# Optimization experiments

Hardware: AMD Instinct MI355X
Metric: run time of the kernel (lower is better)

The kernel has to match this reference:

```python
import jax, jax.numpy as jnp
import numpy as np

GAMMA = 2.0  # init arg gamma
EPS = 1e-8   # torch F.cosine_similarity eps


def setup_inputs() -> dict:
    key = jax.random.key(0)
    k1, k2, k3 = jax.random.split(key, 3)
    B, C, H, W_ = 4, 256, 64, 64
    x = jax.random.normal(k1, (B, C, H, W_), dtype=jnp.float32)
    # 1x1 conv weight [out_c, in_c] and bias
    W = jax.random.normal(k2, (C, C), dtype=jnp.float32) * (1.0 / np.sqrt(C))
    b = jax.random.normal(k3, (C,), dtype=jnp.float32) * 0.01
    return {"x": x, "W": W, "b": b}


def reference(x, W, b):
    B, C, H, W_ = x.shape
    N = H * W_
    xf = x.reshape(B, C, N)                                    # [B,C,N]
    # cosine similarity across channel dim, with torch-style eps clamp
    norm = jnp.maximum(jnp.sqrt(jnp.sum(xf * xf, axis=1)), EPS)  # [B,N]
    xn = xf / norm[:, None, :]                                  # [B,C,N]
    sim = jnp.einsum('bcn,bcm->bnm', xn, xn)                    # [B,N,N]
    sim = jax.nn.relu(sim) ** GAMMA
    # 1x1 conv = per-pixel channel mixing
    t = jnp.einsum('oc,bchw->bohw', W, x) + b[None, :, None, None]
    tf = t.reshape(B, C, N)                                     # [B,C,N]
    # einsum 'b x y h w, b c h w -> b c x y'
    out = jnp.einsum('bnm,bcm->bcn', sim, tf)
    return out.reshape(B, C, H, W_)
```

## Files before the change

kernel.cpp:

```cpp
#include <hip/hip_runtime.h>
#include <stdint.h>

#define CC 256
#define NN 4096

typedef __attribute__((ext_vector_type(8))) short short8;
typedef __attribute__((ext_vector_type(4))) float floatx4;
typedef __attribute__((ext_vector_type(4))) unsigned int uint4v;

__device__ __forceinline__ unsigned short f2bf(float f) {
    unsigned int u = __builtin_bit_cast(unsigned int, f);
    u = (u + 0x7FFFu + ((u >> 16) & 1u)) >> 16;
    return (unsigned short)u;
}

__device__ __forceinline__ floatx4 mfma16(short8 a, short8 b, floatx4 c) {
    return __builtin_amdgcn_mfma_f32_16x16x32_bf16(a, b, c, 0, 0, 0);
}


__global__ __launch_bounds__(256) void k_trans(const float* __restrict__ x,
                                               unsigned short* __restrict__ xB,
                                               unsigned short* __restrict__ xG,
                                               float* __restrict__ psum) {
    int blk = blockIdx.x;
    int b  = blk >> 8;
    int cc = (blk >> 6) & 3;
    int nc = blk & 63;
    int c0 = cc << 6, n0 = nc << 6;
    __shared__ float tile[64][65];
    __shared__ float red[4][64];
    int t = threadIdx.x;
    {
        int c   = t >> 2;
        int nn4 = (t & 3) << 4;
        const float* src = x + (size_t)(b * CC + c0 + c) * NN + n0 + nn4;
        #pragma unroll
        for (int j = 0; j < 16; j += 4) {
            floatx4 v = *(const floatx4*)(src + j);
            tile[c][nn4 + j + 0] = v[0];
            tile[c][nn4 + j + 1] = v[1];
            tile[c][nn4 + j + 2] = v[2];
            tile[c][nn4 + j + 3] = v[3];
        }
    }
    __syncthreads();
    int g = t >> 6, lane = t & 63, l15 = lane & 15, q = lane >> 4;
    #pragma unroll
    for (int kkl = 0; kkl < 2; ++kkl) {
        unsigned int w[4];
        #pragma unroll
        for (int j = 0; j < 4; ++j) {
            unsigned int lo = f2bf(tile[32 * kkl + 8 * q + 2 * j][16 * g + l15]);
            unsigned int hi = f2bf(tile[32 * kkl + 8 * q + 2 * j + 1][16 * g + l15]);
            w[j] = lo | (hi << 16);
        }
        uint4v p = {w[0], w[1], w[2], w[3]};
        *(uint4v*)(xB + ((size_t)(b * 256 + (n0 >> 4) + g) * 8 + (c0 >> 5) + kkl) * 512
                   + lane * 8) = p;
    }
    #pragma unroll
    for (int kk2 = 0; kk2 < 2; ++kk2) {
        unsigned int w[4];
        #pragma unroll
        for (int j = 0; j < 4; ++j) {
            unsigned int lo = f2bf(tile[16 * g + l15][32 * kk2 + 8 * q + 2 * j]);
            unsigned int hi = f2bf(tile[16 * g + l15][32 * kk2 + 8 * q + 2 * j + 1]);
            w[j] = lo | (hi << 16);
        }
        uint4v p = {w[0], w[1], w[2], w[3]};
        *(uint4v*)(xG + (size_t)(b * 64 + nc) * 16 * 1024
                   + ((size_t)((c0 >> 4) + g)) * 1024 + kk2 * 512 + lane * 8) = p;
    }
    {
        int n  = t & 63;
        int cq = t >> 6;
        float ss = 0.f;
        #pragma unroll
        for (int i = 0; i < 16; ++i) {
            float v = tile[cq * 16 + i][n];
            ss = fmaf(v, v, ss);
        }
        red[cq][n] = ss;
    }
    __syncthreads();
    if (t < 64) {
        float s = red[0][t] + red[1][t] + red[2][t] + red[3][t];
        psum[((size_t)(b * 64 + nc) * 64 + t) * 4 + cc] = s;
    }
}

__global__ __launch_bounds__(256) void k_invwcast(const float* __restrict__ psum,
                                                  float* __restrict__ invn,
                                                  const float* __restrict__ Wm,
                                                  unsigned short* __restrict__ wF) {
    int bid = blockIdx.x;
    int t = threadIdx.x;
    if (bid < 64) {
        int i = bid * 256 + t;
        floatx4 p = *(const floatx4*)(psum + (size_t)i * 4);
        float ss = (p[0] + p[1]) + (p[2] + p[3]);
        invn[i] = 1.f / fmaxf(sqrtf(ss), 1e-8f);
    } else {
        int idx = (bid - 64) * 256 + t;
        int f = idx >> 6, lane = idx & 63;
        int ct = f >> 3, kk = f & 7;
        int l15 = lane & 15, q = lane >> 4;
        const float* src = Wm + (size_t)(16 * ct + l15) * CC + 32 * kk + 8 * q;
        floatx4 a = *(const floatx4*)src;
        floatx4 c = *(const floatx4*)(src + 4);
        unsigned int w0 = f2bf(a[0]) | ((unsigned int)f2bf(a[1]) << 16);
        unsigned int w1 = f2bf(a[2]) | ((unsigned int)f2bf(a[3]) << 16);
        unsigned int w2 = f2bf(c[0]) | ((unsigned int)f2bf(c[1]) << 16);
        unsigned int w3 = f2bf(c[2]) | ((unsigned int)f2bf(c[3]) << 16);
        uint4v p = {w0, w1, w2, w3};
        *(uint4v*)(wF + (size_t)f * 512 + lane * 8) = p;
    }
}

#define FUSED_STEP(IT, BQC, BQN, PB)                                           \
    {                                                                          \
        int m0 = (IT) << 6;                                                    \
        int itn = ((IT) < 63) ? (IT) + 1 : 63;                                 \
                       \
        _Pragma("unroll")                                                      \
        for (int kk = 0; kk < 8; ++kk)                                         \
            BQN[kk] = *(const short8*)(xBb                                     \
                + ((size_t)(itn * 4 + ms) * 8 + kk) * 512 + lane * 8);         \
                        \
        short8 xg00, xg01, xg10, xg11;                                         \
        xg00 = *(const short8*)(xGb + (size_t)((IT) * 16 + wv) * 1024          \
                                + 0 * 512 + lane * 8);                         \
        xg01 = *(const short8*)(xGb + (size_t)((IT) * 16 + wv) * 1024          \
                                + 1 * 512 + lane * 8);                         \
        xg10 = *(const short8*)(xGb + (size_t)((IT) * 16 + wv + 8) * 1024      \
                                + 0 * 512 + lane * 8);                         \
        xg11 = *(const short8*)(xGb + (size_t)((IT) * 16 + wv + 8) * 1024      \
                                + 1 * 512 + lane * 8);                         \
        float invm = invb[m0 + 16 * ms + l15];                                 \
                                \
        floatx4 s0a = zero4, s0b = zero4, s1a = zero4, s1b = zero4;            \
        _Pragma("unroll")                                                      \
        for (int kk = 0; kk < 8; kk += 2) {                                    \
            s0a = mfma16(aq[0][kk],     BQC[kk],     s0a);                     \
            s1a = mfma16(aq[1][kk],     BQC[kk],     s1a);                     \
            s0b = mfma16(aq[0][kk + 1], BQC[kk + 1], s0b);                     \
            s1b = mfma16(aq[1][kk + 1], BQC[kk + 1], s1b);                     \
        }                                                                      \
                           \
        _Pragma("unroll")                                                      \
        for (int s = 0; s < 2; ++s) {                                          \
            floatx4 sv = (s == 0) ? (s0a + s0b) : (s1a + s1b);                 \
            unsigned short* pw = PB + (16 * (2 * np + s)) * 72 + 16 * ms + l15;\
            _Pragma("unroll")                                                  \
            for (int i = 0; i < 4; ++i) {                                      \
                float v = sv[i] * (invq[s][i] * invm);                         \
                v = fmaxf(v, 0.f);                                             \
                v = v * v;                                                     \
                csum[s][i] += v;                                               \
                pw[(q * 4 + i) * 72] = f2bf(v);                                \
            }                                                                  \
        }                                                                      \
        asm volatile("s_waitcnt lgkmcnt(0)\n\ts_barrier" ::: "memory");        \
                                                       \
        _Pragma("unroll")                                                      \
        for (int nqs = 0; nqs < 4; ++nqs) {                                    \
            short8 p0 = *(const short8*)(PB + (16 * nqs + l15) * 72 + q * 8);  \
            short8 p1 = *(const short8*)(PB + (16 * nqs + l15) * 72 + 32 + q * 8); \
            Zacc[0][nqs] = mfma16(xg00, p0, Zacc[0][nqs]);                     \
            Zacc[1][nqs] = mfma16(xg10, p0, Zacc[1][nqs]);                     \
            Zacc[0][nqs] = mfma16(xg01, p1, Zacc[0][nqs]);                     \
            Zacc[1][nqs] = mfma16(xg11, p1, Zacc[1][nqs]);                     \
        }                                                                      \
    }

__global__ __launch_bounds__(512, 1) void k_fused(
        const unsigned short* __restrict__ xB,
        const unsigned short* __restrict__ xG,
        const unsigned short* __restrict__ wF,
        const float* __restrict__ bias,
        const float* __restrict__ invn,
        float* __restrict__ out) {
    int blk = blockIdx.x;
    int b  = blk >> 6;
    int n0 = (blk & 63) << 6;
    int t  = threadIdx.x;
    int wv = t >> 6, lane = t & 63;
    int l15 = lane & 15, q = lane >> 4;
    int ms = wv & 3;
    int np = wv >> 2;

    __shared__ unsigned short pbuf[2][64 * 72];
    __shared__ unsigned short zbuf[64 * 264];
    __shared__ float spbuf2[4][64];

    const unsigned short* xBb = xB + (size_t)b * 256 * 8 * 512;
    const unsigned short* xGb = xG + (size_t)b * 64 * 16 * 1024;
    const float* invb = invn + b * NN;

    short8 aq[2][8];
    #pragma unroll
    for (int s = 0; s < 2; ++s)
        #pragma unroll
        for (int kk = 0; kk < 8; ++kk)
            aq[s][kk] = *(const short8*)(xBb
                + ((size_t)((n0 >> 4) + 2 * np + s) * 8 + kk) * 512 + lane * 8);
    float invq[2][4];
    #pragma unroll
    for (int s = 0; s < 2; ++s)
        #pragma unroll
        for (int i = 0; i < 4; ++i)
            invq[s][i] = invb[n0 + 16 * (2 * np + s) + q * 4 + i];

    floatx4 zero4 = {0.f, 0.f, 0.f, 0.f};
    floatx4 Zacc[2][4];
    #pragma unroll
    for (int ci = 0; ci < 2; ++ci)
        #pragma unroll
        for (int nqs = 0; nqs < 4; ++nqs) Zacc[ci][nqs] = zero4;
    float csum[2][4];
    #pragma unroll
    for (int s = 0; s < 2; ++s)
        #pragma unroll
        for (int i = 0; i < 4; ++i) csum[s][i] = 0.f;

    short8 bqA[8], bqB[8];
    #pragma unroll
    for (int kk = 0; kk < 8; ++kk)
        bqA[kk] = *(const short8*)(xBb + ((size_t)(0 * 4 + ms) * 8 + kk) * 512 + lane * 8);

    for (int it2 = 0; it2 < 32; ++it2) {
        int itE = 2 * it2;
        FUSED_STEP(itE,     bqA, bqB, (pbuf[0]));
        int itO = 2 * it2 + 1;
        FUSED_STEP(itO,     bqB, bqA, (pbuf[1]));
    }

    #pragma unroll
    for (int mask = 1; mask < 16; mask <<= 1)
        #pragma unroll
        for (int s = 0; s < 2; ++s)
            #pragma unroll
            for (int i = 0; i < 4; ++i)
                csum[s][i] += __shfl_xor(csum[s][i], mask, 64);

    __syncthreads();
    #pragma unroll
    for (int ci = 0; ci < 2; ++ci) {
        int cct = wv + 8 * ci;
        #pragma unroll
        for (int nqs = 0; nqs < 4; ++nqs)
            #pragma unroll
            for (int i = 0; i < 4; ++i)
                zbuf[(16 * nqs + l15) * 264 + 16 * cct + 4 * q + i] = f2bf(Zacc[ci][nqs][i]);
    }
    if (l15 == 0) {
        #pragma unroll
        for (int s = 0; s < 2; ++s)
            #pragma unroll
            for (int i = 0; i < 4; ++i)
                spbuf2[ms][16 * (2 * np + s) + 4 * q + i] = csum[s][i];
    }
    __syncthreads();

    float svals[4];
    #pragma unroll
    for (int nqs = 0; nqs < 4; ++nqs)
        svals[nqs] = spbuf2[0][16 * nqs + l15] + spbuf2[1][16 * nqs + l15]
                   + spbuf2[2][16 * nqs + l15] + spbuf2[3][16 * nqs + l15];

    float* ob = out + (size_t)b * CC * NN;
    floatx4 oa[2][4];
    #pragma unroll
    for (int ci = 0; ci < 2; ++ci) {
        int ct = wv + 8 * ci;
        floatx4 bv = *(const floatx4*)(bias + 16 * ct + 4 * q);
        #pragma unroll
        for (int nqs = 0; nqs < 4; ++nqs)
            #pragma unroll
            for (int i = 0; i < 4; ++i) oa[ci][nqs][i] = bv[i] * svals[nqs];
    }
    #pragma unroll
    for (int kk = 0; kk < 8; ++kk) {
        short8 wf0 = *(const short8*)(wF + (size_t)(wv * 8 + kk) * 512 + lane * 8);
        short8 wf1 = *(const short8*)(wF + (size_t)((wv + 8) * 8 + kk) * 512 + lane * 8);
        #pragma unroll
        for (int nqs = 0; nqs < 4; ++nqs) {
            short8 zf = *(const short8*)(&zbuf[(16 * nqs + l15) * 264 + 32 * kk + 8 * q]);
            oa[0][nqs] = mfma16(wf0, zf, oa[0][nqs]);
            oa[1][nqs] = mfma16(wf1, zf, oa[1][nqs]);
        }
    }
    #pragma unroll
    for (int ci = 0; ci < 2; ++ci) {
        int ct = wv + 8 * ci;
        #pragma unroll
        for (int nqs = 0; nqs < 4; ++nqs)
            #pragma unroll
            for (int i = 0; i < 4; ++i)
                ob[(size_t)(16 * ct + 4 * q + i) * NN + n0 + 16 * nqs + l15] = oa[ci][nqs][i];
    }
}

extern "C" void kernel_launch(void* const* d_in, const int* in_sizes, int n_in,
                              void* d_out, int out_size, void* d_ws, size_t ws_size,
                              hipStream_t stream) {
    const float* x    = (const float*)d_in[0];
    const float* Wm   = (const float*)d_in[1];
    const float* bias = (const float*)d_in[2];
    float* out = (float*)d_out;

    char* ws = (char*)d_ws;
    float* psum         = (float*)ws;
    float* invn         = (float*)(ws + 262144);
    unsigned short* xB  = (unsigned short*)(ws + 262144 + 65536);
    unsigned short* xG  = (unsigned short*)(ws + 262144 + 65536 + 8388608);
    unsigned short* wF  = (unsigned short*)(ws + 262144 + 65536 + 2 * 8388608);

    k_trans   <<<1024, 256, 0, stream>>>(x, xB, xG, psum);
    k_invwcast<<<96,   256, 0, stream>>>(psum, invn, Wm, wF);
    k_fused   <<<256,  512, 0, stream>>>(xB, xG, wF, bias, invn, out);
}
```

Measured before the change: 165.3 us.

## Halve fused-kernel query tile to 32 pixels with 4-wave blocks, two blocks per CU

```diff
diff --git a/kernel.cpp b/kernel.cpp
--- a/kernel.cpp
+++ b/kernel.cpp
@@ -7,6 +7,7 @@
 typedef __attribute__((ext_vector_type(8))) short short8;
 typedef __attribute__((ext_vector_type(4))) float floatx4;
 typedef __attribute__((ext_vector_type(4))) unsigned int uint4v;
+typedef __attribute__((ext_vector_type(2))) unsigned int uint2v;
 
 __device__ __forceinline__ unsigned short f2bf(float f) {
     unsigned int u = __builtin_bit_cast(unsigned int, f);
@@ -128,15 +129,14 @@
             BQN[kk] = *(const short8*)(xBb                                     \
                 + ((size_t)(itn * 4 + ms) * 8 + kk) * 512 + lane * 8);         \
                         \
-        short8 xg00, xg01, xg10, xg11;                                         \
-        xg00 = *(const short8*)(xGb + (size_t)((IT) * 16 + wv) * 1024          \
-                                + 0 * 512 + lane * 8);                         \
-        xg01 = *(const short8*)(xGb + (size_t)((IT) * 16 + wv) * 1024          \
-                                + 1 * 512 + lane * 8);                         \
-        xg10 = *(const short8*)(xGb + (size_t)((IT) * 16 + wv + 8) * 1024      \
-                                + 0 * 512 + lane * 8);                         \
-        xg11 = *(const short8*)(xGb + (size_t)((IT) * 16 + wv + 8) * 1024      \
-                                + 1 * 512 + lane * 8);                         \
+        short8 xg[4][2];                                                       \
+        _Pragma("unroll")                                                      \
+        for (int ci = 0; ci < 4; ++ci)                                         \
+            _Pragma("unroll")                                                  \
+            for (int kk2 = 0; kk2 < 2; ++kk2)                                  \
+                xg[ci][kk2] = *(const short8*)(xGb                             \
+                    + (size_t)((IT) * 16 + wv + 4 * ci) * 1024                 \
+                    + kk2 * 512 + lane * 8);                                   \
         float invm = invb[m0 + 16 * ms + l15];                                 \
                                 \
         floatx4 s0a = zero4, s0b = zero4, s1a = zero4, s1b = zero4;            \
@@ -151,7 +151,7 @@
         _Pragma("unroll")                                                      \
         for (int s = 0; s < 2; ++s) {                                          \
             floatx4 sv = (s == 0) ? (s0a + s0b) : (s1a + s1b);                 \
-            unsigned short* pw = PB + (16 * (2 * np + s)) * 72 + 16 * ms + l15;\
+            unsigned short* pw = PB + (16 * s) * 72 + 16 * ms + l15;           \
             _Pragma("unroll")                                                  \
             for (int i = 0; i < 4; ++i) {                                      \
                 float v = sv[i] * (invq[s][i] * invm);                         \
@@ -164,17 +164,19 @@
         asm volatile("s_waitcnt lgkmcnt(0)\n\ts_barrier" ::: "memory");        \
                                                        \
         _Pragma("unroll")                                                      \
-        for (int nqs = 0; nqs < 4; ++nqs) {                                    \
-            short8 p0 = *(const short8*)(PB + (16 * nqs + l15) * 72 + q * 8);  \
-            short8 p1 = *(const short8*)(PB + (16 * nqs + l15) * 72 + 32 + q * 8); \
-            Zacc[0][nqs] = mfma16(xg00, p0, Zacc[0][nqs]);                     \
-            Zacc[1][nqs] = mfma16(xg10, p0, Zacc[1][nqs]);                     \
-            Zacc[0][nqs] = mfma16(xg01, p1, Zacc[0][nqs]);                     \
-            Zacc[1][nqs] = mfma16(xg11, p1, Zacc[1][nqs]);                     \
-        }                                                                      \
-    }
-
-__global__ __launch_bounds__(512, 1) void k_fused(
+        for (int kk2 = 0; kk2 < 2; ++kk2)                                      \
+            _Pragma("unroll")                                                  \
+            for (int nqs = 0; nqs < 2; ++nqs) {                                \
+                short8 pbf = *(const short8*)(PB + (16 * nqs + l15) * 72       \
+                                              + kk2 * 32 + q * 8);             \
+                Zacc[0][nqs] = mfma16(xg[0][kk2], pbf, Zacc[0][nqs]);          \
+                Zacc[1][nqs] = mfma16(xg[1][kk2], pbf, Zacc[1][nqs]);          \
+                Zacc[2][nqs] = mfma16(xg[2][kk2], pbf, Zacc[2][nqs]);          \
+                Zacc[3][nqs] = mfma16(xg[3][kk2], pbf, Zacc[3][nqs]);          \
+            }                                                                  \
+    }
+
+__global__ __launch_bounds__(256, 2) void k_fused(
         const unsigned short* __restrict__ xB,
         const unsigned short* __restrict__ xG,
         const unsigned short* __restrict__ wF,
@@ -182,17 +184,16 @@
         const float* __restrict__ invn,
         float* __restrict__ out) {
     int blk = blockIdx.x;
-    int b  = blk >> 6;
-    int n0 = (blk & 63) << 6;
+    int b  = blk >> 7;
+    int n0 = (blk & 127) << 5;
     int t  = threadIdx.x;
     int wv = t >> 6, lane = t & 63;
     int l15 = lane & 15, q = lane >> 4;
-    int ms = wv & 3;
-    int np = wv >> 2;
-
-    __shared__ unsigned short pbuf[2][64 * 72];
-    __shared__ unsigned short zbuf[64 * 264];
-    __shared__ float spbuf2[4][64];
+    int ms = wv;
+
+    __shared__ unsigned short pbuf[2][32 * 72];
+    __shared__ unsigned short zbuf[32 * 264];
+    __shared__ float spbuf2[4][32];
 
     const unsigned short* xBb = xB + (size_t)b * 256 * 8 * 512;
     const unsigned short* xGb = xG + (size_t)b * 64 * 16 * 1024;
@@ -204,20 +205,20 @@
         #pragma unroll
         for (int kk = 0; kk < 8; ++kk)
             aq[s][kk] = *(const short8*)(xBb
-                + ((size_t)((n0 >> 4) + 2 * np + s) * 8 + kk) * 512 + lane * 8);
+                + ((size_t)((n0 >> 4) + s) * 8 + kk) * 512 + lane * 8);
     float invq[2][4];
     #pragma unroll
     for (int s = 0; s < 2; ++s)
         #pragma unroll
         for (int i = 0; i < 4; ++i)
-            invq[s][i] = invb[n0 + 16 * (2 * np + s) + q * 4 + i];
+            invq[s][i] = invb[n0 + 16 * s + q * 4 + i];
 
     floatx4 zero4 = {0.f, 0.f, 0.f, 0.f};
-    floatx4 Zacc[2][4];
-    #pragma unroll
-    for (int ci = 0; ci < 2; ++ci)
-        #pragma unroll
-        for (int nqs = 0; nqs < 4; ++nqs) Zacc[ci][nqs] = zero4;
+    floatx4 Zacc[4][2];
+    #pragma unroll
+    for (int ci = 0; ci < 4; ++ci)
+        #pragma unroll
+        for (int nqs = 0; nqs < 2; ++nqs) Zacc[ci][nqs] = zero4;
     float csum[2][4];
     #pragma unroll
     for (int s = 0; s < 2; ++s)
@@ -227,13 +228,13 @@
     short8 bqA[8], bqB[8];
     #pragma unroll
     for (int kk = 0; kk < 8; ++kk)
-        bqA[kk] = *(const short8*)(xBb + ((size_t)(0 * 4 + ms) * 8 + kk) * 512 + lane * 8);
+        bqA[kk] = *(const short8*)(xBb + ((size_t)(ms) * 8 + kk) * 512 + lane * 8);
 
     for (int it2 = 0; it2 < 32; ++it2) {
         int itE = 2 * it2;
-        FUSED_STEP(itE,     bqA, bqB, (pbuf[0]));
+        FUSED_STEP(itE, bqA, bqB, (pbuf[0]));
         int itO = 2 * it2 + 1;
-        FUSED_STEP(itO,     bqB, bqA, (pbuf[1]));
+        FUSED_STEP(itO, bqB, bqA, (pbuf[1]));
     }
 
     #pragma unroll
@@ -246,56 +247,59 @@
 
     __syncthreads();
     #pragma unroll
-    for (int ci = 0; ci < 2; ++ci) {
-        int cct = wv + 8 * ci;
-        #pragma unroll
-        for (int nqs = 0; nqs < 4; ++nqs)
-            #pragma unroll
-            for (int i = 0; i < 4; ++i)
-                zbuf[(16 * nqs + l15) * 264 + 16 * cct + 4 * q + i] = f2bf(Zacc[ci][nqs][i]);
+    for (int ci = 0; ci < 4; ++ci) {
+        int ct = wv + 4 * ci;
+        #pragma unroll
+        for (int nqs = 0; nqs < 2; ++nqs) {
+            unsigned int lo = f2bf(Zacc[ci][nqs][0]) | ((unsigned int)f2bf(Zacc[ci][nqs][1]) << 16);
+            unsigned int hi = f2bf(Zacc[ci][nqs][2]) | ((unsigned int)f2bf(Zacc[ci][nqs][3]) << 16);
+            uint2v pz = {lo, hi};
+            *(uint2v*)(&zbuf[(16 * nqs + l15) * 264 + 16 * ct + 4 * q]) = pz;
+        }
     }
     if (l15 == 0) {
         #pragma unroll
         for (int s = 0; s < 2; ++s)
             #pragma unroll
             for (int i = 0; i < 4; ++i)
-                spbuf2[ms][16 * (2 * np + s) + 4 * q + i] = csum[s][i];
+                spbuf2[ms][16 * s + 4 * q + i] = csum[s][i];
     }
     __syncthreads();
 
-    float svals[4];
-    #pragma unroll
-    for (int nqs = 0; nqs < 4; ++nqs)
+    float svals[2];
+    #pragma unroll
+    for (int nqs = 0; nqs < 2; ++nqs)
         svals[nqs] = spbuf2[0][16 * nqs + l15] + spbuf2[1][16 * nqs + l15]
                    + spbuf2[2][16 * nqs + l15] + spbuf2[3][16 * nqs + l15];
 
     float* ob = out + (size_t)b * CC * NN;
-    floatx4 oa[2][4];
-    #pragma unroll
-    for (int ci = 0; ci < 2; ++ci) {
-        int ct = wv + 8 * ci;
+    floatx4 oa[4][2];
+    #pragma unroll
+    for (int ci = 0; ci < 4; ++ci) {
+        int ct = wv + 4 * ci;
         floatx4 bv = *(const floatx4*)(bias + 16 * ct + 4 * q);
         #pragma unroll
-        for (int nqs = 0; nqs < 4; ++nqs)
+        for (int nqs = 0; nqs < 2; ++nqs)
             #pragma unroll
             for (int i = 0; i < 4; ++i) oa[ci][nqs][i] = bv[i] * svals[nqs];
     }
     #pragma unroll
     for (int kk = 0; kk < 8; ++kk) {
-        short8 wf0 = *(const short8*)(wF + (size_t)(wv * 8 + kk) * 512 + lane * 8);
-        short8 wf1 = *(const short8*)(wF + (size_t)((wv + 8) * 8 + kk) * 512 + lane * 8);
-        #pragma unroll
-        for (int nqs = 0; nqs < 4; ++nqs) {
-            short8 zf = *(const short8*)(&zbuf[(16 * nqs + l15) * 264 + 32 * kk + 8 * q]);
-            oa[0][nqs] = mfma16(wf0, zf, oa[0][nqs]);
-            oa[1][nqs] = mfma16(wf1, zf, oa[1][nqs]);
-        }
-    }
-    #pragma unroll
-    for (int ci = 0; ci < 2; ++ci) {
-        int ct = wv + 8 * ci;
-        #pragma unroll
-        for (int nqs = 0; nqs < 4; ++nqs)
+        short8 zf0 = *(const short8*)(&zbuf[(l15) * 264 + 32 * kk + 8 * q]);
+        short8 zf1 = *(const short8*)(&zbuf[(16 + l15) * 264 + 32 * kk + 8 * q]);
+        #pragma unroll
+        for (int ci = 0; ci < 4; ++ci) {
+            int ct = wv + 4 * ci;
+            short8 wf = *(const short8*)(wF + (size_t)(ct * 8 + kk) * 512 + lane * 8);
+            oa[ci][0] = mfma16(wf, zf0, oa[ci][0]);
+            oa[ci][1] = mfma16(wf, zf1, oa[ci][1]);
+        }
+    }
+    #pragma unroll
+    for (int ci = 0; ci < 4; ++ci) {
+        int ct = wv + 4 * ci;
+        #pragma unroll
+        for (int nqs = 0; nqs < 2; ++nqs)
             #pragma unroll
             for (int i = 0; i < 4; ++i)
                 ob[(size_t)(16 * ct + 4 * q + i) * NN + n0 + 16 * nqs + l15] = oa[ci][nqs][i];
@@ -319,5 +323,5 @@
 
     k_trans   <<<1024, 256, 0, stream>>>(x, xB, xG, psum);
     k_invwcast<<<96,   256, 0, stream>>>(psum, invn, Wm, wF);
-    k_fused   <<<256,  512, 0, stream>>>(xB, xG, wF, bias, invn, out);
-}
+    k_fused   <<<512,  256, 0, stream>>>(xB, xG, wF, bias, invn, out);
+}
```

Result: slower. 171.0 us (+3.4%).

## Software-pipeline the P·X accumulation one step behind and transpose the sim tile

Applied to the files above, without the earlier changes.

```diff
diff --git a/kernel.cpp b/kernel.cpp
--- a/kernel.cpp
+++ b/kernel.cpp
@@ -7,6 +7,7 @@
 typedef __attribute__((ext_vector_type(8))) short short8;
 typedef __attribute__((ext_vector_type(4))) float floatx4;
 typedef __attribute__((ext_vector_type(4))) unsigned int uint4v;
+typedef __attribute__((ext_vector_type(2))) unsigned int uint2v;
 
 __device__ __forceinline__ unsigned short f2bf(float f) {
     unsigned int u = __builtin_bit_cast(unsigned int, f);
@@ -118,60 +119,70 @@
     }
 }
 
-#define FUSED_STEP(IT, BQC, BQN, PB)                                           \
+#define FUSED_STEP(IT, BQC, BQN, XGP, XGC, DO_G2)                              \
     {                                                                          \
-        int m0 = (IT) << 6;                                                    \
-        int itn = ((IT) < 63) ? (IT) + 1 : 63;                                 \
-                       \
+                \
         _Pragma("unroll")                                                      \
         for (int kk = 0; kk < 8; ++kk)                                         \
-            BQN[kk] = *(const short8*)(xBb                                     \
-                + ((size_t)(itn * 4 + ms) * 8 + kk) * 512 + lane * 8);         \
-                        \
-        short8 xg00, xg01, xg10, xg11;                                         \
-        xg00 = *(const short8*)(xGb + (size_t)((IT) * 16 + wv) * 1024          \
-                                + 0 * 512 + lane * 8);                         \
-        xg01 = *(const short8*)(xGb + (size_t)((IT) * 16 + wv) * 1024          \
-                                + 1 * 512 + lane * 8);                         \
-        xg10 = *(const short8*)(xGb + (size_t)((IT) * 16 + wv + 8) * 1024      \
-                                + 0 * 512 + lane * 8);                         \
-        xg11 = *(const short8*)(xGb + (size_t)((IT) * 16 + wv + 8) * 1024      \
-                                + 1 * 512 + lane * 8);                         \
-        float invm = invb[m0 + 16 * ms + l15];                                 \
-                                \
+            BQN[kk] = *(const short8*)(bqp + kk * 512);                        \
+        bqp += 16384;                                                          \
+        _Pragma("unroll")                                                      \
+        for (int ci = 0; ci < 2; ++ci)                                         \
+            _Pragma("unroll")                                                  \
+            for (int kk2 = 0; kk2 < 2; ++kk2)                                  \
+                XGC[ci][kk2] = *(const short8*)(xgp + ci * 8192 + kk2 * 512);  \
+        xgp += 16384;                                                          \
+        floatx4 invm4 = *(const floatx4*)invmp;                                \
+        invmp += 64;                                                           \
+                                       \
+        if (DO_G2) {                                                           \
+            const unsigned short* pbR = pbuf[((IT) - 1) & 1];                  \
+            _Pragma("unroll")                                                  \
+            for (int kk2 = 0; kk2 < 2; ++kk2)                                  \
+                _Pragma("unroll")                                              \
+                for (int nqs = 0; nqs < 4; ++nqs) {                            \
+                    short8 pbf = *(const short8*)(pbR + (16 * nqs + l15) * 72  \
+                                                  + kk2 * 32 + q * 8);         \
+                    Zacc[0][nqs] = mfma16(XGP[0][kk2], pbf, Zacc[0][nqs]);     \
+                    Zacc[1][nqs] = mfma16(XGP[1][kk2], pbf, Zacc[1][nqs]);     \
+                }                                                              \
+        }                                                                      \
+                  \
         floatx4 s0a = zero4, s0b = zero4, s1a = zero4, s1b = zero4;            \
         _Pragma("unroll")                                                      \
         for (int kk = 0; kk < 8; kk += 2) {                                    \
-            s0a = mfma16(aq[0][kk],     BQC[kk],     s0a);                     \
-            s1a = mfma16(aq[1][kk],     BQC[kk],     s1a);                     \
-            s0b = mfma16(aq[0][kk + 1], BQC[kk + 1], s0b);                     \
-            s1b = mfma16(aq[1][kk + 1], BQC[kk + 1], s1b);                     \
+            s0a = mfma16(BQC[kk],     aq[0][kk],     s0a);                     \
+            s1a = mfma16(BQC[kk],     aq[1][kk],     s1a);                     \
+            s0b = mfma16(BQC[kk + 1], aq[0][kk + 1], s0b);                     \
+            s1b = mfma16(BQC[kk + 1], aq[1][kk + 1], s1b);                     \
         }                                                                      \
-                           \
-        _Pragma("unroll")                                                      \
-        for (int s = 0; s < 2; ++s) {                                          \
-            floatx4 sv = (s == 0) ? (s0a + s0b) : (s1a + s1b);                 \
-            unsigned short* pw = PB + (16 * (2 * np + s)) * 72 + 16 * ms + l15;\
+                  \
+        {                                                                      \
+            unsigned short* pbW = pbuf[(IT) & 1];                              \
             _Pragma("unroll")                                                  \
-            for (int i = 0; i < 4; ++i) {                                      \
-                float v = sv[i] * (invq[s][i] * invm);                         \
-                v = fmaxf(v, 0.f);                                             \
-                v = v * v;                                                     \
-                csum[s][i] += v;                                               \
-                pw[(q * 4 + i) * 72] = f2bf(v);                                \
+            for (int s = 0; s < 2; ++s) {                                      \
+                floatx4 sv = (s == 0) ? (s0a + s0b) : (s1a + s1b);             \
+                unsigned int pk0, pk1;                                         \
+                float v0 = sv[0] * (invm4[0] * invq[s]);                       \
+                float v1 = sv[1] * (invm4[1] * invq[s]);                       \
+                float v2 = sv[2] * (invm4[2] * invq[s]);                       \
+                float v3 = sv[3] * (invm4[3] * invq[s]);                       \
+                v0 = fmaxf(v0, 0.f); v1 = fmaxf(v1, 0.f);                      \
+                v2 = fmaxf(v2, 0.f); v3 = fmaxf(v3, 0.f);                      \
+                v0 *= v0; v1 *= v1; v2 *= v2; v3 *= v3;                        \
+                csum[s] += (v0 + v1) + (v2 + v3);                              \
+                pk0 = __byte_perm(__builtin_bit_cast(unsigned int, v0) + 0x8000u, \
+                                  __builtin_bit_cast(unsigned int, v1) + 0x8000u, \
+                                  0x7632);                                     \
+                pk1 = __byte_perm(__builtin_bit_cast(unsigned int, v2) + 0x8000u, \
+                                  __builtin_bit_cast(unsigned int, v3) + 0x8000u, \
+                                  0x7632);                                     \
+                uint2v w2 = {pk0, pk1};                                        \
+                *(uint2v*)(pbW + (16 * (2 * np + s) + l15) * 72                \
+                           + 16 * ms + 4 * q) = w2;                            \
             }                                                                  \
         }                                                                      \
         asm volatile("s_waitcnt lgkmcnt(0)\n\ts_barrier" ::: "memory");        \
-                                                       \
-        _Pragma("unroll")                                                      \
-        for (int nqs = 0; nqs < 4; ++nqs) {                                    \
-            short8 p0 = *(const short8*)(PB + (16 * nqs + l15) * 72 + q * 8);  \
-            short8 p1 = *(const short8*)(PB + (16 * nqs + l15) * 72 + 32 + q * 8); \
-            Zacc[0][nqs] = mfma16(xg00, p0, Zacc[0][nqs]);                     \
-            Zacc[1][nqs] = mfma16(xg10, p0, Zacc[1][nqs]);                     \
-            Zacc[0][nqs] = mfma16(xg01, p1, Zacc[0][nqs]);                     \
-            Zacc[1][nqs] = mfma16(xg11, p1, Zacc[1][nqs]);                     \
-        }                                                                      \
     }
 
 __global__ __launch_bounds__(512, 1) void k_fused(
@@ -205,12 +216,9 @@
         for (int kk = 0; kk < 8; ++kk)
             aq[s][kk] = *(const short8*)(xBb
                 + ((size_t)((n0 >> 4) + 2 * np + s) * 8 + kk) * 512 + lane * 8);
-    float invq[2][4];
-    #pragma unroll
-    for (int s = 0; s < 2; ++s)
-        #pragma unroll
-        for (int i = 0; i < 4; ++i)
-            invq[s][i] = invb[n0 + 16 * (2 * np + s) + q * 4 + i];
+    float invq[2];
+    #pragma unroll
+    for (int s = 0; s < 2; ++s) invq[s] = invb[n0 + 16 * (2 * np + s) + l15];
 
     floatx4 zero4 = {0.f, 0.f, 0.f, 0.f};
     floatx4 Zacc[2][4];
@@ -218,31 +226,45 @@
     for (int ci = 0; ci < 2; ++ci)
         #pragma unroll
         for (int nqs = 0; nqs < 4; ++nqs) Zacc[ci][nqs] = zero4;
-    float csum[2][4];
-    #pragma unroll
-    for (int s = 0; s < 2; ++s)
-        #pragma unroll
-        for (int i = 0; i < 4; ++i) csum[s][i] = 0.f;
+    float csum[2] = {0.f, 0.f};
+
+    const unsigned short* bqp   = xBb + ms * 4096 + lane * 8;
+    const unsigned short* xgp   = xGb + wv * 1024 + lane * 8;
+    const float*          invmp = invb + 16 * ms + 4 * q;
 
     short8 bqA[8], bqB[8];
+    short8 xgA[2][2], xgB[2][2];
     #pragma unroll
     for (int kk = 0; kk < 8; ++kk)
-        bqA[kk] = *(const short8*)(xBb + ((size_t)(0 * 4 + ms) * 8 + kk) * 512 + lane * 8);
-
-    for (int it2 = 0; it2 < 32; ++it2) {
-        int itE = 2 * it2;
-        FUSED_STEP(itE,     bqA, bqB, (pbuf[0]));
+        bqA[kk] = *(const short8*)(bqp + kk * 512);
+    bqp += 16384;
+
+    FUSED_STEP(0, bqA, bqB, xgB, xgA, false)
+    for (int it2 = 0; it2 < 31; ++it2) {
         int itO = 2 * it2 + 1;
-        FUSED_STEP(itO,     bqB, bqA, (pbuf[1]));
-    }
-
-    #pragma unroll
-    for (int mask = 1; mask < 16; mask <<= 1)
-        #pragma unroll
-        for (int s = 0; s < 2; ++s)
+        FUSED_STEP(itO, bqB, bqA, xgA, xgB, true)
+        int itE = 2 * it2 + 2;
+        FUSED_STEP(itE, bqA, bqB, xgB, xgA, true)
+    }
+    FUSED_STEP(63, bqB, bqA, xgA, xgB, true)
+    {
+        const unsigned short* pbR = pbuf[1];
+        #pragma unroll
+        for (int kk2 = 0; kk2 < 2; ++kk2)
             #pragma unroll
-            for (int i = 0; i < 4; ++i)
-                csum[s][i] += __shfl_xor(csum[s][i], mask, 64);
+            for (int nqs = 0; nqs < 4; ++nqs) {
+                short8 pbf = *(const short8*)(pbR + (16 * nqs + l15) * 72
+                                              + kk2 * 32 + q * 8);
+                Zacc[0][nqs] = mfma16(xgB[0][kk2], pbf, Zacc[0][nqs]);
+                Zacc[1][nqs] = mfma16(xgB[1][kk2], pbf, Zacc[1][nqs]);
+            }
+    }
+
+    #pragma unroll
+    for (int s = 0; s < 2; ++s) {
+        csum[s] += __shfl_xor(csum[s], 16, 64);
+        csum[s] += __shfl_xor(csum[s], 32, 64);
+    }
 
     __syncthreads();
     #pragma unroll
@@ -254,12 +276,10 @@
             for (int i = 0; i < 4; ++i)
                 zbuf[(16 * nqs + l15) * 264 + 16 * cct + 4 * q + i] = f2bf(Zacc[ci][nqs][i]);
     }
-    if (l15 == 0) {
+    if (q == 0) {
         #pragma unroll
         for (int s = 0; s < 2; ++s)
-            #pragma unroll
-            for (int i = 0; i < 4; ++i)
-                spbuf2[ms][16 * (2 * np + s) + 4 * q + i] = csum[s][i];
+            spbuf2[ms][16 * (2 * np + s) + l15] = csum[s];
     }
     __syncthreads();
 
```

After: 154.6 us. 6.5% less time.
